# Kernel tuning notes

Measured on AMD Instinct MI355X. Metric: run time of the kernel, lower is better.

The kernel has to match this reference:

```python
import jax, jax.numpy as jnp
import numpy as np

BN_EPS = 1e-5


def setup_inputs() -> dict:
    key = jax.random.key(0)
    k1, k2, k3 = jax.random.split(key, 3)
    B, IN, H, C = 65536, 784, 1024, 10
    x = jax.random.normal(k1, (B, IN), dtype=jnp.float32)
    # Kaiming-ish real-valued latent weights
    w1 = jax.random.normal(k2, (H, IN), dtype=jnp.float32) * 0.03
    w2 = jax.random.normal(k3, (C, H), dtype=jnp.float32) * 0.03
    gamma = jnp.ones((H,), dtype=jnp.float32)
    beta = jnp.zeros((H,), dtype=jnp.float32)
    return {"x": x, "w1": w1, "w2": w2, "gamma": gamma, "beta": beta}


def _bin_weight(w):
    # XNOR-Net weight binarization: per-output-row alpha * sign(w)
    alpha = jnp.mean(jnp.abs(w), axis=1, keepdims=True)  # [out, 1]
    return alpha * jnp.sign(w)


def reference(x, w1, w2, gamma, beta):
    x = x.reshape(x.shape[0], -1)                      # [B, 784]
    h = x @ _bin_weight(w1).T                          # [B, 1024]
    # BatchNorm1d, training mode: batch mean / biased variance
    mu = jnp.mean(h, axis=0)
    var = jnp.mean(jnp.square(h - mu), axis=0)
    h = gamma * (h - mu) * jax.lax.rsqrt(var + BN_EPS) + beta
    a = jnp.sign(h)                                    # binarized activation
    out = a @ _bin_weight(w2).T                        # [B, 10]
    return out
```

## Files before the change

kernel.cpp:

```cpp
#include <hip/hip_runtime.h>
#include <hip/hip_fp16.h>

#define BATCH   65536
#define IN_DIM  784
#define KH      800
#define NSTEP   25
#define H_DIM   1024
#define C_DIM   10
#define BN_EPS  1e-5f
#define SLOT    24576

typedef _Float16 half8 __attribute__((ext_vector_type(8)));
typedef float    f32x4 __attribute__((ext_vector_type(4)));

#if defined(__has_builtin)
#if __has_builtin(__builtin_amdgcn_global_load_lds)
#define HAVE_ASYNC 1
#endif
#endif
#ifndef HAVE_ASYNC
#define HAVE_ASYNC 0
#endif

__device__ __forceinline__ void stage16(const _Float16* g, _Float16* ldsBase, int lane) {
#if HAVE_ASYNC
  __builtin_amdgcn_global_load_lds((const __attribute__((address_space(1))) void*)g,
                                   (__attribute__((address_space(3))) void*)ldsBase,
                                   16, 0, 0);
#else
  *(half8*)(ldsBase + lane * 8) = *(const half8*)g;
#endif
}

__global__ __launch_bounds__(256) void prep_w(const float* __restrict__ w1,
                                              const float* __restrict__ w2,
                                              float* __restrict__ alpha1,
                                              _Float16* __restrict__ S2,
                                              _Float16* __restrict__ S2W,
                                              float* __restrict__ A2P,
                                              float* __restrict__ colz) {
  __shared__ float red[4];
  const int tid = threadIdx.x, lane = tid & 63, wave = tid >> 6;
  const int j = blockIdx.x;
  if (j < H_DIM) {
    const float* wr = w1 + (long)j * IN_DIM;
    float s = 0.f;
    for (int k = tid; k < IN_DIM; k += 256) s += fabsf(wr[k]);
#pragma unroll
    for (int off = 32; off > 0; off >>= 1) s += __shfl_xor(s, off, 64);
    if (lane == 0) red[wave] = s;
    __syncthreads();
    if (tid == 0) alpha1[j] = (red[0] + red[1] + red[2] + red[3]) * (1.f / IN_DIM);
    _Float16* dr = S2 + (long)j * KH;
    for (int k = tid; k < KH; k += 256) {
      const float v = (k < IN_DIM) ? wr[k] : 0.f;
      dr[k] = (_Float16)((v > 0.f) ? 1.f : ((v < 0.f) ? -1.f : 0.f));
    }
  } else if (j < H_DIM + C_DIM) {
    const int c = j - H_DIM;
    const float* wr = w2 + (long)c * H_DIM;
    float s = 0.f;
    for (int k = tid; k < H_DIM; k += 256) s += fabsf(wr[k]);
#pragma unroll
    for (int off = 32; off > 0; off >>= 1) s += __shfl_xor(s, off, 64);
    if (lane == 0) red[wave] = s;
    __syncthreads();
    if (tid == 0) A2P[c] = (red[0] + red[1] + red[2] + red[3]) * (1.f / H_DIM);
    for (int k = tid; k < H_DIM; k += 256) {
      const float v = wr[k];
      S2W[(long)c * H_DIM + k] = (_Float16)((v > 0.f) ? 1.f : ((v < 0.f) ? -1.f : 0.f));
    }
  } else {
    for (int k = tid; k < 2 * H_DIM; k += 256) colz[k] = 0.f;
    for (int k = tid; k < 6 * H_DIM; k += 256) S2W[10 * H_DIM + k] = (_Float16)0.f;
    if (tid < 6) A2P[10 + tid] = 0.f;
  }
}

__global__ __launch_bounds__(512) void gemm1(const float* __restrict__ x,
                                             const _Float16* __restrict__ S2,
                                             const float* __restrict__ alpha1,
                                             float* __restrict__ H,
                                             float* __restrict__ colsum,
                                             float* __restrict__ colsumsq) {
  __shared__ _Float16 lds[3 * SLOT];
  const int tid  = threadIdx.x;
  const int lane = tid & 63;
  const int w    = tid >> 6;
  const int wr   = w >> 2;
  const int wc   = w & 3;

  const int b     = blockIdx.x;
  const int xcd   = b & 7;
  const int local = b >> 3;
  const long m0   = (long)(xcd * 32 + (local >> 2)) * 256;
  const int  n0   = (local & 3) * 256;

  const int rowS  = tid >> 1;
  const int halfS = tid & 1;
  const float* xp = x + (m0 + rowS) * (long)IN_DIM;
  const int sA = (rowS >> 1) & 3;
  const int c0 = (halfS * 2) ^ sA;
  const int c1 = (halfS * 2 + 1) ^ sA;
  const int aw = rowS * 32;

  const int c8 = ((lane & 3) ^ ((lane >> 3) & 3)) * 8;
  const _Float16* bG = S2 + (long)(n0 + w * 32 + (lane >> 2)) * KH + c8;
  const int ldsW0 = (w * 32) * 32;
  const int ldsW1 = (w * 32 + 16) * 32;

  const int fr = lane & 15;
  const int kc = lane >> 4;
  const int cp = (kc ^ ((fr >> 1) & 3)) * 8;
  const int aoff = (wr * 128 + fr) * 32 + cp;
  const int boff = (wc * 64 + fr) * 32 + cp;

  f32x4 acc[8][4] = {};
  f32x4 rE[4], rO[4];

#define CONV_WRITE(RC, PW, KB) do {                                          \
    const bool vldc = ((KB) + halfS * 16) <= (IN_DIM - 16);                  \
    half8 hh0 = {}, hh1 = {}, hl0 = {}, hl1 = {};                            \
    if (vldc) {                                                              \
      _Pragma("unroll")                                                      \
      for (int i = 0; i < 8; ++i) {                                          \
        const float f0 = (i < 4) ? (RC)[0][i & 3] : (RC)[1][i & 3];          \
        const float f1 = (i < 4) ? (RC)[2][i & 3] : (RC)[3][i & 3];          \
        const _Float16 h0 = (_Float16)f0, h1 = (_Float16)f1;                 \
        hh0[i] = h0; hl0[i] = (_Float16)(f0 - (float)h0);                    \
        hh1[i] = h1; hl1[i] = (_Float16)(f1 - (float)h1);                    \
      }                                                                      \
    }                                                                        \
    *(half8*)((PW) + aw + c0 * 8) = hh0;                                     \
    *(half8*)((PW) + aw + c1 * 8) = hh1;                                     \
    *(half8*)((PW) + 8192 + aw + c0 * 8) = hl0;                              \
    *(half8*)((PW) + 8192 + aw + c1 * 8) = hl1;                              \
  } while (0)

#define ALOAD(RL, KL) do {                                                   \
    if (((KL) + halfS * 16) <= (IN_DIM - 16)) {                              \
      const float* src = xp + (KL) + halfS * 16;                             \
      (RL)[0] = *(const f32x4*)(src);                                        \
      (RL)[1] = *(const f32x4*)(src + 4);                                    \
      (RL)[2] = *(const f32x4*)(src + 8);                                    \
      (RL)[3] = *(const f32x4*)(src + 12);                                   \
    } else {                                                                 \
      (RL)[0] = f32x4{}; (RL)[1] = f32x4{}; (RL)[2] = f32x4{}; (RL)[3] = f32x4{}; \
    }                                                                        \
  } while (0)

#define GSTEP(T, RLOAD, RCONV, DO_STAGE, DO_LOAD, VM) do {                   \
    asm volatile("s_waitcnt vmcnt(" #VM ")" ::: "memory");                   \
    __builtin_amdgcn_s_barrier();                                            \
    asm volatile("" ::: "memory");                                           \
    _Float16* Scur = &lds[((T) % 3) * SLOT];                                 \
    if (DO_STAGE) {                                                          \
      _Float16* Pw = &lds[(((T) + 2) % 3) * SLOT];                           \
      const int kb = ((T) + 2) * 32;                                         \
      stage16(bG + kb,           Pw + 16384 + ldsW0, lane);                  \
      stage16(bG + 16 * KH + kb, Pw + 16384 + ldsW1, lane);                  \
      if (DO_LOAD) { ALOAD(RLOAD, ((T) + 3) * 32); }                         \
      CONV_WRITE(RCONV, Pw, kb);                                             \
    }                                                                        \
    half8 af[8], bf[4];                                                      \
    _Pragma("unroll")                                                        \
    for (int ni = 0; ni < 4; ++ni) bf[ni] = *(const half8*)&Scur[16384 + boff + ni * 512]; \
    _Pragma("unroll")                                                        \
    for (int mi = 0; mi < 8; ++mi) af[mi] = *(const half8*)&Scur[aoff + mi * 512]; \
    __builtin_amdgcn_s_setprio(1);                                           \
    _Pragma("unroll")                                                        \
    for (int mi = 0; mi < 8; ++mi)                                           \
      _Pragma("unroll")                                                      \
      for (int ni = 0; ni < 4; ++ni)                                         \
        acc[mi][ni] = __builtin_amdgcn_mfma_f32_16x16x32_f16(af[mi], bf[ni], acc[mi][ni], 0, 0, 0); \
    __builtin_amdgcn_s_setprio(0);                                           \
    _Pragma("unroll")                                                        \
    for (int mi = 0; mi < 8; ++mi) af[mi] = *(const half8*)&Scur[8192 + aoff + mi * 512]; \
    __builtin_amdgcn_s_setprio(1);                                           \
    _Pragma("unroll")                                                        \
    for (int mi = 0; mi < 8; ++mi)                                           \
      _Pragma("unroll")                                                      \
      for (int ni = 0; ni < 4; ++ni)                                         \
        acc[mi][ni] = __builtin_amdgcn_mfma_f32_16x16x32_f16(af[mi], bf[ni], acc[mi][ni], 0, 0, 0); \
    __builtin_amdgcn_s_setprio(0);                                           \
  } while (0)

  stage16(bG + 0,                 lds + 16384 + ldsW0, lane);
  stage16(bG + 16 * KH + 0,       lds + 16384 + ldsW1, lane);
  stage16(bG + 32,                lds + SLOT + 16384 + ldsW0, lane);
  stage16(bG + 16 * KH + 32,      lds + SLOT + 16384 + ldsW1, lane);
  {
    f32x4 rt[4];
    ALOAD(rt, 0);
    CONV_WRITE(rt, (&lds[0]), 0);
    ALOAD(rt, 32);
    CONV_WRITE(rt, (&lds[SLOT]), 32);
  }
  ALOAD(rO, 64);
  asm volatile("s_waitcnt lgkmcnt(0)" ::: "memory");

  for (int tp = 0; tp < 11; ++tp) {
    const int t0 = tp * 2;
    GSTEP(t0,     rE, rO, 1, 1, 6);
    GSTEP(t0 + 1, rO, rE, 1, 1, 6);
  }
  GSTEP(22, rE, rO, 1, 0, 6);
  GSTEP(23, rE, rO, 0, 0, 6);
  GSTEP(24, rE, rO, 0, 0, 0);

  asm volatile("s_waitcnt vmcnt(0)" ::: "memory");

  const int rq = (lane >> 4) * 4;
#pragma unroll
  for (int ni = 0; ni < 4; ++ni) {
    const int col = n0 + wc * 64 + ni * 16 + fr;
    const float a1 = alpha1[col];
    float s = 0.f, q = 0.f;
#pragma unroll
    for (int mi = 0; mi < 8; ++mi) {
#pragma unroll
      for (int r = 0; r < 4; ++r) {
        const long row = m0 + wr * 128 + mi * 16 + rq + r;
        const float v = acc[mi][ni][r] * a1;
        H[row * H_DIM + col] = v;
        s += v;
        q += v * v;
      }
    }
    s += __shfl_xor(s, 16, 64);
    s += __shfl_xor(s, 32, 64);
    q += __shfl_xor(q, 16, 64);
    q += __shfl_xor(q, 32, 64);
    if ((lane >> 4) == 0) {
      atomicAdd(&colsum[col], s);
      atomicAdd(&colsumsq[col], q);
    }
  }
#undef GSTEP
#undef ALOAD
#undef CONV_WRITE
}

__global__ __launch_bounds__(256) void final_k(const float* __restrict__ H,
                                               const float* __restrict__ colsum,
                                               const float* __restrict__ colsumsq,
                                               const float* __restrict__ gamma,
                                               const float* __restrict__ beta,
                                               const _Float16* __restrict__ S2W,
                                               const float* __restrict__ A2P,
                                               float* __restrict__ out) {
  __shared__ _Float16 bs[16 * H_DIM];
  __shared__ float cs[H_DIM], ts[H_DIM];
  const int tid = threadIdx.x, lane = tid & 63, wave = tid >> 6;

  {
    const int j = tid * 4;
    const f32x4 s  = *(const f32x4*)&colsum[j];
    const f32x4 q  = *(const f32x4*)&colsumsq[j];
    const f32x4 g  = *(const f32x4*)&gamma[j];
    const f32x4 bt = *(const f32x4*)&beta[j];
    f32x4 c, t;
#pragma unroll
    for (int i = 0; i < 4; ++i) {
      const float mu  = s[i] * (1.f / BATCH);
      const float var = q[i] * (1.f / BATCH) - mu * mu;
      c[i] = g[i] * rsqrtf(var + BN_EPS);
      t[i] = bt[i] - c[i] * mu;
    }
    *(f32x4*)&cs[j] = c;
    *(f32x4*)&ts[j] = t;
  }
  for (int i = tid; i < 2048; i += 256) {
    const int oc = i >> 7, cc = i & 127;
    *(half8*)&bs[oc * H_DIM + ((cc ^ (oc & 7)) << 3)] = *(const half8*)&S2W[oc * H_DIM + (cc << 3)];
  }
  __syncthreads();

  const int lr = lane & 15, lg = lane >> 4;
  const float alf = A2P[lr];
  const long r0 = ((long)blockIdx.x * 4 + wave) * 16;
  const float* hp = H + (r0 + lr) * H_DIM + lg * 8;

  f32x4 acc = {};
#pragma unroll 4
  for (int ks = 0; ks < 32; ++ks) {
    const f32x4 h0 = *(const f32x4*)(hp + ks * 32);
    const f32x4 h1 = *(const f32x4*)(hp + ks * 32 + 4);
    const int jb = ks * 32 + lg * 8;
    const f32x4 c0v = *(const f32x4*)&cs[jb];
    const f32x4 c1v = *(const f32x4*)&cs[jb + 4];
    const f32x4 t0v = *(const f32x4*)&ts[jb];
    const f32x4 t1v = *(const f32x4*)&ts[jb + 4];
    half8 afr;
#pragma unroll
    for (int i = 0; i < 4; ++i) {
      const float hv = h0[i] * c0v[i] + t0v[i];
      afr[i] = (_Float16)((hv > 0.f) ? 1.f : ((hv < 0.f) ? -1.f : 0.f));
    }
#pragma unroll
    for (int i = 0; i < 4; ++i) {
      const float hv = h1[i] * c1v[i] + t1v[i];
      afr[4 + i] = (_Float16)((hv > 0.f) ? 1.f : ((hv < 0.f) ? -1.f : 0.f));
    }
    const int cc = (ks * 4 + lg) ^ (lr & 7);
    const half8 bfr = *(const half8*)&bs[lr * H_DIM + cc * 8];
    acc = __builtin_amdgcn_mfma_f32_16x16x32_f16(afr, bfr, acc, 0, 0, 0);
  }

  __syncthreads();
  float* outs = (float*)bs;
  if (lr < C_DIM) {
#pragma unroll
    for (int r = 0; r < 4; ++r)
      outs[(wave * 16 + lg * 4 + r) * C_DIM + lr] = acc[r] * alf;
  }
  __syncthreads();
  if (tid < 160)
    *(f32x4*)&out[(long)blockIdx.x * 640 + tid * 4] = *(const f32x4*)&outs[tid * 4];
}

extern "C" void kernel_launch(void* const* d_in, const int* in_sizes, int n_in,
                              void* d_out, int out_size, void* d_ws, size_t ws_size,
                              hipStream_t stream) {
  const float* x     = (const float*)d_in[0];
  const float* w1    = (const float*)d_in[1];
  const float* w2    = (const float*)d_in[2];
  const float* gamma = (const float*)d_in[3];
  const float* beta  = (const float*)d_in[4];
  float* out = (float*)d_out;

  char* ws = (char*)d_ws;
  float*    H      = (float*)   (ws + 0);
  _Float16* S2     = (_Float16*)(ws + 268435456LL);
  _Float16* S2W    = (_Float16*)(ws + 270073856LL);
  float*    ALPHA1 = (float*)   (ws + 270106624LL);
  float*    A2P    = (float*)   (ws + 270110720LL);
  float*    COLS   = (float*)   (ws + 270110976LL);
  float*    COLQ   = (float*)   (ws + 270115072LL);

  prep_w<<<H_DIM + C_DIM + 1, 256, 0, stream>>>(w1, w2, ALPHA1, S2, S2W, A2P, COLS);
  gemm1<<<1024, 512, 0, stream>>>(x, S2, ALPHA1, H, COLS, COLQ);
  final_k<<<BATCH / 64, 256, 0, stream>>>(H, COLS, COLQ, gamma, beta, S2W, A2P, out);
}
```

Measured before the change: 580.8 us.

## Halve gemm1 M tile to 128 and switch to simpler double-buffered pipeline

The first GEMM's row tile shrinks from 256 to 128 and the grid doubles to 2048 blocks. Each block uses a two-slot LDS buffer of 64 KB instead of three 48 KB slots, so more blocks can fit per CU. The deep software pipeline with register double-buffering of x loads is replaced by a simple loop that loads one step ahead and waits on vmcnt(0) every step. This trades lower per-block latency hiding and twice the B-tile re-reads for higher occupancy and fewer live registers.

```diff
diff --git a/kernel.cpp b/kernel.cpp
--- a/kernel.cpp
+++ b/kernel.cpp
@@ -8,7 +8,7 @@
 #define H_DIM   1024
 #define C_DIM   10
 #define BN_EPS  1e-5f
-#define SLOT    24576
+#define SLOTH   16384
 
 typedef _Float16 half8 __attribute__((ext_vector_type(8)));
 typedef float    f32x4 __attribute__((ext_vector_type(4)));
@@ -83,7 +83,7 @@
                                              float* __restrict__ H,
                                              float* __restrict__ colsum,
                                              float* __restrict__ colsumsq) {
-  __shared__ _Float16 lds[3 * SLOT];
+  __shared__ _Float16 lds[2 * SLOTH];
   const int tid  = threadIdx.x;
   const int lane = tid & 63;
   const int w    = tid >> 6;
@@ -93,15 +93,13 @@
   const int b     = blockIdx.x;
   const int xcd   = b & 7;
   const int local = b >> 3;
-  const long m0   = (long)(xcd * 32 + (local >> 2)) * 256;
+  const long m0   = (long)(xcd * 64 + (local >> 2)) * 128;
   const int  n0   = (local & 3) * 256;
 
-  const int rowS  = tid >> 1;
-  const int halfS = tid & 1;
+  const int rowS = tid >> 2;
+  const int q    = tid & 3;
   const float* xp = x + (m0 + rowS) * (long)IN_DIM;
-  const int sA = (rowS >> 1) & 3;
-  const int c0 = (halfS * 2) ^ sA;
-  const int c1 = (halfS * 2 + 1) ^ sA;
+  const int cq = (q ^ ((rowS >> 1) & 3)) * 8;
   const int aw = rowS * 32;
 
   const int c8 = ((lane & 3) ^ ((lane >> 3) & 3)) * 8;
@@ -112,101 +110,80 @@
   const int fr = lane & 15;
   const int kc = lane >> 4;
   const int cp = (kc ^ ((fr >> 1) & 3)) * 8;
-  const int aoff = (wr * 128 + fr) * 32 + cp;
+  const int aoff = (wr * 64 + fr) * 32 + cp;
   const int boff = (wc * 64 + fr) * 32 + cp;
 
-  f32x4 acc[8][4] = {};
-  f32x4 rE[4], rO[4];
-
-#define CONV_WRITE(RC, PW, KB) do {                                          \
-    const bool vldc = ((KB) + halfS * 16) <= (IN_DIM - 16);                  \
-    half8 hh0 = {}, hh1 = {}, hl0 = {}, hl1 = {};                            \
-    if (vldc) {                                                              \
+  f32x4 acc[4][4] = {};
+
+#define ALOAD(R0, R1, KB) do {                                               \
+    if (((KB) + q * 8) <= (IN_DIM - 8)) {                                    \
+      const float* src = xp + (KB) + q * 8;                                  \
+      (R0) = *(const f32x4*)(src);                                           \
+      (R1) = *(const f32x4*)(src + 4);                                       \
+    } else { (R0) = f32x4{}; (R1) = f32x4{}; }                               \
+  } while (0)
+
+#define CONV_WRITE(R0, R1, PW, KB) do {                                      \
+    half8 hh = {}, hl = {};                                                  \
+    if (((KB) + q * 8) <= (IN_DIM - 8)) {                                    \
       _Pragma("unroll")                                                      \
       for (int i = 0; i < 8; ++i) {                                          \
-        const float f0 = (i < 4) ? (RC)[0][i & 3] : (RC)[1][i & 3];          \
-        const float f1 = (i < 4) ? (RC)[2][i & 3] : (RC)[3][i & 3];          \
-        const _Float16 h0 = (_Float16)f0, h1 = (_Float16)f1;                 \
-        hh0[i] = h0; hl0[i] = (_Float16)(f0 - (float)h0);                    \
-        hh1[i] = h1; hl1[i] = (_Float16)(f1 - (float)h1);                    \
+        const float f = (i < 4) ? (R0)[i] : (R1)[i & 3];                     \
+        const _Float16 h = (_Float16)f;                                      \
+        hh[i] = h; hl[i] = (_Float16)(f - (float)h);                         \
       }                                                                      \
     }                                                                        \
-    *(half8*)((PW) + aw + c0 * 8) = hh0;                                     \
-    *(half8*)((PW) + aw + c1 * 8) = hh1;                                     \
-    *(half8*)((PW) + 8192 + aw + c0 * 8) = hl0;                              \
-    *(half8*)((PW) + 8192 + aw + c1 * 8) = hl1;                              \
+    *(half8*)((PW) + aw + cq) = hh;                                          \
+    *(half8*)((PW) + 4096 + aw + cq) = hl;                                   \
   } while (0)
 
-#define ALOAD(RL, KL) do {                                                   \
-    if (((KL) + halfS * 16) <= (IN_DIM - 16)) {                              \
-      const float* src = xp + (KL) + halfS * 16;                             \
-      (RL)[0] = *(const f32x4*)(src);                                        \
-      (RL)[1] = *(const f32x4*)(src + 4);                                    \
-      (RL)[2] = *(const f32x4*)(src + 8);                                    \
-      (RL)[3] = *(const f32x4*)(src + 12);                                   \
-    } else {                                                                 \
-      (RL)[0] = f32x4{}; (RL)[1] = f32x4{}; (RL)[2] = f32x4{}; (RL)[3] = f32x4{}; \
-    }                                                                        \
-  } while (0)
-
-#define GSTEP(T, RLOAD, RCONV, DO_STAGE, DO_LOAD, VM) do {                   \
-    asm volatile("s_waitcnt vmcnt(" #VM ")" ::: "memory");                   \
-    __builtin_amdgcn_s_barrier();                                            \
-    asm volatile("" ::: "memory");                                           \
-    _Float16* Scur = &lds[((T) % 3) * SLOT];                                 \
-    if (DO_STAGE) {                                                          \
-      _Float16* Pw = &lds[(((T) + 2) % 3) * SLOT];                           \
-      const int kb = ((T) + 2) * 32;                                         \
-      stage16(bG + kb,           Pw + 16384 + ldsW0, lane);                  \
-      stage16(bG + 16 * KH + kb, Pw + 16384 + ldsW1, lane);                  \
-      if (DO_LOAD) { ALOAD(RLOAD, ((T) + 3) * 32); }                         \
-      CONV_WRITE(RCONV, Pw, kb);                                             \
-    }                                                                        \
-    half8 af[8], bf[4];                                                      \
-    _Pragma("unroll")                                                        \
-    for (int ni = 0; ni < 4; ++ni) bf[ni] = *(const half8*)&Scur[16384 + boff + ni * 512]; \
-    _Pragma("unroll")                                                        \
-    for (int mi = 0; mi < 8; ++mi) af[mi] = *(const half8*)&Scur[aoff + mi * 512]; \
-    __builtin_amdgcn_s_setprio(1);                                           \
-    _Pragma("unroll")                                                        \
-    for (int mi = 0; mi < 8; ++mi)                                           \
-      _Pragma("unroll")                                                      \
-      for (int ni = 0; ni < 4; ++ni)                                         \
-        acc[mi][ni] = __builtin_amdgcn_mfma_f32_16x16x32_f16(af[mi], bf[ni], acc[mi][ni], 0, 0, 0); \
-    __builtin_amdgcn_s_setprio(0);                                           \
-    _Pragma("unroll")                                                        \
-    for (int mi = 0; mi < 8; ++mi) af[mi] = *(const half8*)&Scur[8192 + aoff + mi * 512]; \
-    __builtin_amdgcn_s_setprio(1);                                           \
-    _Pragma("unroll")                                                        \
-    for (int mi = 0; mi < 8; ++mi)                                           \
-      _Pragma("unroll")                                                      \
-      for (int ni = 0; ni < 4; ++ni)                                         \
-        acc[mi][ni] = __builtin_amdgcn_mfma_f32_16x16x32_f16(af[mi], bf[ni], acc[mi][ni], 0, 0, 0); \
-    __builtin_amdgcn_s_setprio(0);                                           \
-  } while (0)
-
-  stage16(bG + 0,                 lds + 16384 + ldsW0, lane);
-  stage16(bG + 16 * KH + 0,       lds + 16384 + ldsW1, lane);
-  stage16(bG + 32,                lds + SLOT + 16384 + ldsW0, lane);
-  stage16(bG + 16 * KH + 32,      lds + SLOT + 16384 + ldsW1, lane);
+  stage16(bG + 0,           lds + 8192 + ldsW0, lane);
+  stage16(bG + 16 * KH + 0, lds + 8192 + ldsW1, lane);
   {
-    f32x4 rt[4];
-    ALOAD(rt, 0);
-    CONV_WRITE(rt, (&lds[0]), 0);
-    ALOAD(rt, 32);
-    CONV_WRITE(rt, (&lds[SLOT]), 32);
-  }
-  ALOAD(rO, 64);
-  asm volatile("s_waitcnt lgkmcnt(0)" ::: "memory");
-
-  for (int tp = 0; tp < 11; ++tp) {
-    const int t0 = tp * 2;
-    GSTEP(t0,     rE, rO, 1, 1, 6);
-    GSTEP(t0 + 1, rO, rE, 1, 1, 6);
-  }
-  GSTEP(22, rE, rO, 1, 0, 6);
-  GSTEP(23, rE, rO, 0, 0, 6);
-  GSTEP(24, rE, rO, 0, 0, 0);
+    f32x4 r0, r1;
+    ALOAD(r0, r1, 0);
+    asm volatile("s_waitcnt vmcnt(0)" ::: "memory");
+    CONV_WRITE(r0, r1, (&lds[0]), 0);
+  }
+
+  for (int t = 0; t < NSTEP; ++t) {
+    _Float16* Scur = &lds[(t & 1) * SLOTH];
+    _Float16* Pw   = &lds[((t + 1) & 1) * SLOTH];
+    const int kb = ((t + 1 < NSTEP) ? (t + 1) : (NSTEP - 1)) * 32;
+
+    asm volatile("s_waitcnt lgkmcnt(0)" ::: "memory");
+    __builtin_amdgcn_s_barrier();
+    asm volatile("" ::: "memory");
+
+    stage16(bG + kb,           Pw + 8192 + ldsW0, lane);
+    stage16(bG + 16 * KH + kb, Pw + 8192 + ldsW1, lane);
+    f32x4 r0, r1;
+    ALOAD(r0, r1, kb);
+
+    half8 afh[4], afl[4], bf[4];
+#pragma unroll
+    for (int ni = 0; ni < 4; ++ni) bf[ni] = *(const half8*)&Scur[8192 + boff + ni * 512];
+#pragma unroll
+    for (int mi = 0; mi < 4; ++mi) afh[mi] = *(const half8*)&Scur[aoff + mi * 512];
+#pragma unroll
+    for (int mi = 0; mi < 4; ++mi) afl[mi] = *(const half8*)&Scur[4096 + aoff + mi * 512];
+
+    __builtin_amdgcn_s_setprio(1);
+#pragma unroll
+    for (int mi = 0; mi < 4; ++mi)
+#pragma unroll
+      for (int ni = 0; ni < 4; ++ni)
+        acc[mi][ni] = __builtin_amdgcn_mfma_f32_16x16x32_f16(afh[mi], bf[ni], acc[mi][ni], 0, 0, 0);
+#pragma unroll
+    for (int mi = 0; mi < 4; ++mi)
+#pragma unroll
+      for (int ni = 0; ni < 4; ++ni)
+        acc[mi][ni] = __builtin_amdgcn_mfma_f32_16x16x32_f16(afl[mi], bf[ni], acc[mi][ni], 0, 0, 0);
+    __builtin_amdgcn_s_setprio(0);
+
+    asm volatile("s_waitcnt vmcnt(0)" ::: "memory");
+    CONV_WRITE(r0, r1, Pw, kb);
+  }
 
   asm volatile("s_waitcnt vmcnt(0)" ::: "memory");
 
@@ -215,28 +192,27 @@
   for (int ni = 0; ni < 4; ++ni) {
     const int col = n0 + wc * 64 + ni * 16 + fr;
     const float a1 = alpha1[col];
-    float s = 0.f, q = 0.f;
-#pragma unroll
-    for (int mi = 0; mi < 8; ++mi) {
+    float s = 0.f, qq = 0.f;
+#pragma unroll
+    for (int mi = 0; mi < 4; ++mi) {
 #pragma unroll
       for (int r = 0; r < 4; ++r) {
-        const long row = m0 + wr * 128 + mi * 16 + rq + r;
+        const long row = m0 + wr * 64 + mi * 16 + rq + r;
         const float v = acc[mi][ni][r] * a1;
         H[row * H_DIM + col] = v;
         s += v;
-        q += v * v;
+        qq += v * v;
       }
     }
     s += __shfl_xor(s, 16, 64);
     s += __shfl_xor(s, 32, 64);
-    q += __shfl_xor(q, 16, 64);
-    q += __shfl_xor(q, 32, 64);
+    qq += __shfl_xor(qq, 16, 64);
+    qq += __shfl_xor(qq, 32, 64);
     if ((lane >> 4) == 0) {
       atomicAdd(&colsum[col], s);
-      atomicAdd(&colsumsq[col], q);
-    }
-  }
-#undef GSTEP
+      atomicAdd(&colsumsq[col], qq);
+    }
+  }
 #undef ALOAD
 #undef CONV_WRITE
 }
@@ -339,6 +315,6 @@
   float*    COLQ   = (float*)   (ws + 270115072LL);
 
   prep_w<<<H_DIM + C_DIM + 1, 256, 0, stream>>>(w1, w2, ALPHA1, S2, S2W, A2P, COLS);
-  gemm1<<<1024, 512, 0, stream>>>(x, S2, ALPHA1, H, COLS, COLQ);
+  gemm1<<<2048, 512, 0, stream>>>(x, S2, ALPHA1, H, COLS, COLQ);
   final_k<<<BATCH / 64, 256, 0, stream>>>(H, COLS, COLQ, gamma, beta, S2W, A2P, out);
 }
```

New measurement: 586.8 us. About the same (+1.0%).
